# Kernel optimization log

Measured on AMD Instinct MI355X. Metric: run time of the kernel, lower is better.

## Reference

```python
import jax, jax.numpy as jnp
import numpy as np

NEURON_CDECAY = 0.5
NEURON_VDECAY = 0.75
NEURON_VTH = 0.5
SPIKE_WINDOW = 0.5


@jax.custom_vjp
def pseudo_spike(v):
    return (v > NEURON_VTH).astype(v.dtype)

def _ps_fwd(v):
    return pseudo_spike(v), v

def _ps_bwd(v, g):
    return (g * (jnp.abs(v - NEURON_VTH) < SPIKE_WINDOW).astype(g.dtype),)

pseudo_spike.defvjp(_ps_fwd, _ps_bwd)


def setup_inputs() -> dict:
    key = jax.random.key(0)
    ks = jax.random.split(key, 6)
    B, S, T, H, A = 4096, 256, 50, 256, 2
    # NCP mask with fanout=256 over 256 targets selects every target -> dense.
    x = jax.random.uniform(ks[0], (B, S, T), dtype=jnp.float32)
    w1 = jax.random.normal(ks[1], (S, H), dtype=jnp.float32)
    w2 = jax.random.normal(ks[2], (H, H), dtype=jnp.float32)
    w3 = jax.random.normal(ks[3], (H, H), dtype=jnp.float32)
    w4 = jax.random.normal(ks[4], (H, A), dtype=jnp.float32)
    b1 = jnp.zeros((H,), jnp.float32)
    b2 = jnp.zeros((H,), jnp.float32)
    b3 = jnp.zeros((H,), jnp.float32)
    b4 = jnp.zeros((A,), jnp.float32)
    return {"x": x, "w1": w1, "b1": b1, "w2": w2, "b2": b2,
            "w3": w3, "b3": b3, "w4": w4, "b4": b4, "batch_size": B}


def _lif(pre, W, b, u, v, s):
    # torch: linear(pre, weight=W.t(), bias=b) == pre @ W + b  (W is [src, tgt])
    cur = u * NEURON_CDECAY + pre @ W + b
    volt = v * NEURON_VDECAY * (1.0 - s) + cur
    spk = pseudo_spike(volt)
    return cur, volt, spk


def reference(x, w1, b1, w2, b2, w3, b3, w4, b4, batch_size):
    B = x.shape[0]
    T = x.shape[2]
    H1, H2, H3, A = w1.shape[1], w2.shape[1], w3.shape[1], w4.shape[1]
    z = lambda d: jnp.zeros((B, d), x.dtype)
    carry0 = (z(H1), z(H1), z(H1), z(H2), z(H2), z(H2),
              z(H3), z(H3), z(H3), z(A), z(A), z(A))
    xt = jnp.transpose(x, (2, 0, 1))  # [T, B, S]

    def step(carry, inp):
        u1, v1, s1, u2, v2, s2, u3, v3, s3, u4, v4, s4 = carry
        u1, v1, s1 = _lif(inp, w1, b1, u1, v1, s1)
        u2, v2, s2 = _lif(s1, w2, b2, u2, v2, s2)
        u3, v3, s3 = _lif(s2, w3, b3, u3, v3, s3)
        u4, v4, s4 = _lif(s3, w4, b4, u4, v4, s4)
        return (u1, v1, s1, u2, v2, s2, u3, v3, s3, u4, v4, s4), s4

    _, s4_all = jax.lax.scan(step, carry0, xt)  # [T, B, A]
    fc4_sumspike = jnp.sum(s4_all, axis=0) / T
    # faithful to the source: out is divided by batch_window a second time
    out = fc4_sumspike / T
    return out
```

## Files before the change

### kernel.cpp

```cpp
#include <hip/hip_runtime.h>

typedef unsigned short u16;
typedef unsigned int u32;

#define B_N 4096
#define S_N 256
#define T_N 50
#define H_N 256

#define W1F 0
#define W2F 65536
#define W3F 131072
#define W4F 196608
#define B1F 197120
#define B2F 197376
#define B3F 197632
#define B4F 197888
#define CVT_N 197890
#define FLAGI 198656

__device__ __forceinline__ float bf2f(u16 h) { return __uint_as_float(((u32)h) << 16); }
__device__ __forceinline__ u16 f2bf(float f) {
  u32 x = __float_as_uint(f);
  return (u16)((x + 0x7fffu + ((x >> 16) & 1u)) >> 16);
}
__device__ __forceinline__ float ld_f(const void* p, size_t i, int isbf) {
  return isbf ? bf2f(((const u16*)p)[i]) : ((const float*)p)[i];
}

__global__ void detect_dtype(const u16* __restrict__ x, int* __restrict__ flag) {
  __shared__ int cnt[256];
  int c = 0;
  for (int i = threadIdx.x; i < 4096; i += 256) c += (x[2 * i] <= 0x3F80u) ? 1 : 0;
  cnt[threadIdx.x] = c;
  __syncthreads();
  if (threadIdx.x == 0) {
    int tot = 0;
    for (int i = 0; i < 256; i++) tot += cnt[i];
    flag[0] = (tot > 3000) ? 1 : 0;
  }
}

__global__ void convert_inputs(const void* w1, const void* w2, const void* w3,
                               const void* w4, const void* b1, const void* b2,
                               const void* b3, const void* b4, float* __restrict__ ws) {
  const int isbf = ((const int*)ws)[FLAGI];
  int i = blockIdx.x * 256 + threadIdx.x;
  if (i >= CVT_N) return;
  float v;
  if (i < 196608) {
    const void* src = (i < 65536) ? w1 : (i < 131072 ? w2 : w3);
    const int j = i & 65535;
    const int k = j & 3, hp = (j >> 2) & 63, s = j >> 8;
    v = ld_f(src, (size_t)((s << 8) + (k << 6) + hp), isbf);
  } else if (i < 197120) v = ld_f(w4, (size_t)(i - W4F), isbf);
  else if (i < 197376) v = ld_f(b1, (size_t)(i - B1F), isbf);
  else if (i < 197632) v = ld_f(b2, (size_t)(i - B2F), isbf);
  else if (i < 197888) v = ld_f(b3, (size_t)(i - B3F), isbf);
  else v = ld_f(b4, (size_t)(i - B4F), isbf);
  ws[i] = v;
}

template <int OFF, int TN>
__device__ __forceinline__ void gemm_l1(const float4* __restrict__ wp,
                                        const float (*__restrict__ A)[52],
                                        int rdf, float (&acc)[13][4]) {
  const float4* ar0 = (const float4*)(&A[0][rdf]);
  float4 q0 = ar0[0], q1 = ar0[1], q2 = ar0[2], q3 = ar0[3];
  float4 wv = wp[0];
  for (int s = 0; s < S_N; s++) {
    const int sn = (s + 1) & 255;
    const float4* arn = (const float4*)(&A[sn][rdf]);
    float4 p0 = arn[0], p1 = arn[1], p2 = arn[2], p3 = arn[3];
    float4 wn = wp[(size_t)sn << 6];
    const float a[16] = {q0.x, q0.y, q0.z, q0.w, q1.x, q1.y, q1.z, q1.w,
                         q2.x, q2.y, q2.z, q2.w, q3.x, q3.y, q3.z, q3.w};
#pragma unroll
    for (int i = 0; i < TN; i++) {
      acc[i][0] = fmaf(a[OFF + i], wv.x, acc[i][0]);
      acc[i][1] = fmaf(a[OFF + i], wv.y, acc[i][1]);
      acc[i][2] = fmaf(a[OFF + i], wv.z, acc[i][2]);
      acc[i][3] = fmaf(a[OFF + i], wv.w, acc[i][3]);
    }
    q0 = p0; q1 = p1; q2 = p2; q3 = p3; wv = wn;
  }
}

template <int T0, int TN>
__device__ __forceinline__ void gemm_sp(const float4* __restrict__ wp,
                                        const float (*__restrict__ A)[52],
                                        float (&acc)[13][4]) {
  uint2 bv = *(const uint2*)(&A[0][50]);
  float4 wv = wp[0];
  for (int s = 0; s < S_N; s++) {
    const int sn = (s + 1) & 255;
    uint2 bn = *(const uint2*)(&A[sn][50]);
    float4 wn = wp[(size_t)sn << 6];
    const u32 bw0 = (u32)__builtin_amdgcn_readfirstlane((int)bv.x);
    const u32 bw1 = (u32)__builtin_amdgcn_readfirstlane((int)bv.y);
#pragma unroll
    for (int i = 0; i < TN; i++) {
      const int t = T0 + i;
      const u32 bw = (t < 32) ? bw0 : bw1;
      if (bw & (1u << (t & 31))) {
        acc[i][0] += wv.x; acc[i][1] += wv.y; acc[i][2] += wv.z; acc[i][3] += wv.w;
      }
    }
    bv = bn; wv = wn;
  }
}

__device__ __forceinline__ void lif_scan(float (*Af)[52], int tid, float bh) {
  float c[T_N];
  {
    const float4* rr = (const float4*)&Af[tid][0];
#pragma unroll
    for (int j = 0; j < 12; j++) {
      float4 v = rr[j];
      c[4 * j] = v.x; c[4 * j + 1] = v.y; c[4 * j + 2] = v.z; c[4 * j + 3] = v.w;
    }
    float2 v = *(const float2*)&Af[tid][48];
    c[48] = v.x; c[49] = v.y;
  }
  float uu = 0.f, vv = 0.f, ss = 0.f;
  u32 bw0 = 0u, bw1 = 0u;
#pragma unroll
  for (int t = 0; t < T_N; t++) {
    float cur = fmaf(uu, 0.5f, c[t]) + bh;
    float t1 = vv * 0.75f;
    float volt = fmaf(t1, 1.0f - ss, cur);
    bool sp = volt > 0.5f;
    if (t < 32) bw0 |= sp ? (1u << t) : 0u;
    else        bw1 |= sp ? (1u << (t - 32)) : 0u;
    uu = cur; vv = volt; ss = sp ? 1.0f : 0.0f;
  }
  ((u32*)&Af[tid][50])[0] = bw0;
  ((u32*)&Af[tid][50])[1] = bw1;
}

__global__ __launch_bounds__(256, 3) void snn_f32(
    const void* __restrict__ x, const float* __restrict__ ws, void* __restrict__ out) {
  __shared__ float Af[S_N][52];
  __shared__ float z4[T_N][2];

  const int b = blockIdx.x;
  const int tid = threadIdx.x;
  const int isbf = ((const int*)ws)[FLAGI];
  const int tq = tid >> 6;
  const int hp = tid & 63;
  const int t0 = (tq < 2) ? 13 * tq : 26 + 12 * (tq - 2);
  const int tn = (tq < 2) ? 13 : 12;
  const int rdf = 12 * tq;

  {
    const size_t base = ((size_t)b * S_N + tid) * T_N;
    if (isbf) {
      const u32* xr = (const u32*)((const u16*)x + base);
#pragma unroll
      for (int j = 0; j < 25; j++) {
        u32 d = xr[j];
        Af[tid][2 * j] = bf2f((u16)(d & 0xffffu));
        Af[tid][2 * j + 1] = bf2f((u16)(d >> 16));
      }
    } else {
      const float* xf = (const float*)x + base;
#pragma unroll
      for (int j = 0; j < 25; j++) {
        float2 d = *(const float2*)(xf + 2 * j);
        Af[tid][2 * j] = d.x;
        Af[tid][2 * j + 1] = d.y;
      }
    }
  }

  const int WOFF[3] = {W1F, W2F, W3F};
  const int BOFF[3] = {B1F, B2F, B3F};

  for (int l = 0; l < 3; l++) {
    __syncthreads();
    const float4* wp = (const float4*)(ws + WOFF[l]) + hp;

    float acc[13][4];
#pragma unroll
    for (int i = 0; i < 13; i++) {
#pragma unroll
      for (int k = 0; k < 4; k++) acc[i][k] = 0.0f;
    }

    if (l == 0) {
      if (tq == 0)      gemm_l1<0, 13>(wp, Af, 0, acc);
      else if (tq == 1) gemm_l1<1, 13>(wp, Af, 12, acc);
      else if (tq == 2) gemm_l1<2, 12>(wp, Af, 24, acc);
      else              gemm_l1<2, 12>(wp, Af, 36, acc);
    } else {
      if (tq == 0)      gemm_sp<0, 13>(wp, Af, acc);
      else if (tq == 1) gemm_sp<13, 13>(wp, Af, acc);
      else if (tq == 2) gemm_sp<26, 12>(wp, Af, acc);
      else              gemm_sp<38, 12>(wp, Af, acc);
    }
    __syncthreads();

#pragma unroll
    for (int i = 0; i < 13; i++) {
      if (i < tn) {
#pragma unroll
        for (int k = 0; k < 4; k++) Af[hp + 64 * k][t0 + i] = acc[i][k];
      }
    }
    __syncthreads();

    lif_scan(Af, tid, ws[BOFF[l] + tid]);
  }

  __syncthreads();
  if (tid < 2 * T_N) {
    const int t = tid >> 1, a = tid & 1;
    const int wd = t >> 5, bt = t & 31;
    float az = 0.f;
    const float* w4p = ws + W4F + a;
    for (int h = 0; h < H_N; h++) {
      const u32 bits = ((const u32*)&Af[h][50])[wd];
      const float m = (float)((bits >> bt) & 1u);
      az = fmaf(m, w4p[2 * h], az);
    }
    z4[t][a] = az;
  }
  __syncthreads();
  if (tid < 2) {
    const float bh = ws[B4F + tid];
    float uu = 0.f, vv = 0.f, ss = 0.f, sum = 0.f;
    for (int t = 0; t < T_N; t++) {
      float cur = fmaf(uu, 0.5f, z4[t][tid]) + bh;
      float t1 = vv * 0.75f;
      float volt = fmaf(t1, 1.0f - ss, cur);
      float sp = (volt > 0.5f) ? 1.0f : 0.0f;
      uu = cur; vv = volt; ss = sp;
      sum += sp;
    }
    float o = sum / 50.0f / 50.0f;
    if (isbf) ((u16*)out)[b * 2 + tid] = f2bf(o);
    else ((float*)out)[b * 2 + tid] = o;
  }
}

extern "C" void kernel_launch(void* const* d_in, const int* in_sizes, int n_in,
                              void* d_out, int out_size, void* d_ws, size_t ws_size,
                              hipStream_t stream) {
  const void* x  = d_in[0];
  const void* w1 = d_in[1];
  const void* b1 = d_in[2];
  const void* w2 = d_in[3];
  const void* b2 = d_in[4];
  const void* w3 = d_in[5];
  const void* b3 = d_in[6];
  const void* w4 = d_in[7];
  const void* b4 = d_in[8];

  float* ws = (float*)d_ws;
  int* flag = (int*)d_ws + FLAGI;

  detect_dtype<<<1, 256, 0, stream>>>((const u16*)x, flag);
  convert_inputs<<<(CVT_N + 255) / 256, 256, 0, stream>>>(w1, w2, w3, w4, b1, b2, b3, b4, ws);
  snn_f32<<<B_N, 256, 0, stream>>>(x, ws, d_out);
}
```

Baseline: 1.268 ms.

## Use branchless FMA masking in sparse GEMM, keep bf16 input packed, drop manual prefetch

Result: slower. 1.333 ms (+5.1%).

```diff
diff --git a/kernel.cpp b/kernel.cpp
--- a/kernel.cpp
+++ b/kernel.cpp
@@ -61,18 +61,36 @@
   ws[i] = v;
 }
 
+template <int T0, int TN, int WB>
+__device__ __forceinline__ void gemm_l1_bf(const float4* __restrict__ wp,
+                                           const float (*__restrict__ A)[52],
+                                           float (&acc)[13][4]) {
+  for (int s = 0; s < S_N; s++) {
+    const float4 wv = wp[(size_t)s << 6];
+    const uint2* ar = (const uint2*)((const u32*)&A[s][0] + WB);
+    const uint2 r0 = ar[0], r1 = ar[1], r2 = ar[2], r3 = ar[3];
+    const u32 wrd[8] = {r0.x, r0.y, r1.x, r1.y, r2.x, r2.y, r3.x, r3.y};
+#pragma unroll
+    for (int i = 0; i < TN; i++) {
+      const int p = T0 + i - 2 * WB;
+      const u32 w = wrd[p >> 1];
+      const float a = __uint_as_float((p & 1) ? (w & 0xffff0000u) : (w << 16));
+      acc[i][0] = fmaf(a, wv.x, acc[i][0]);
+      acc[i][1] = fmaf(a, wv.y, acc[i][1]);
+      acc[i][2] = fmaf(a, wv.z, acc[i][2]);
+      acc[i][3] = fmaf(a, wv.w, acc[i][3]);
+    }
+  }
+}
+
 template <int OFF, int TN>
-__device__ __forceinline__ void gemm_l1(const float4* __restrict__ wp,
-                                        const float (*__restrict__ A)[52],
-                                        int rdf, float (&acc)[13][4]) {
-  const float4* ar0 = (const float4*)(&A[0][rdf]);
-  float4 q0 = ar0[0], q1 = ar0[1], q2 = ar0[2], q3 = ar0[3];
-  float4 wv = wp[0];
+__device__ __forceinline__ void gemm_l1_f32(const float4* __restrict__ wp,
+                                            const float (*__restrict__ A)[52],
+                                            int rdf, float (&acc)[13][4]) {
   for (int s = 0; s < S_N; s++) {
-    const int sn = (s + 1) & 255;
-    const float4* arn = (const float4*)(&A[sn][rdf]);
-    float4 p0 = arn[0], p1 = arn[1], p2 = arn[2], p3 = arn[3];
-    float4 wn = wp[(size_t)sn << 6];
+    const float4 wv = wp[(size_t)s << 6];
+    const float4* ar = (const float4*)(&A[s][rdf]);
+    const float4 q0 = ar[0], q1 = ar[1], q2 = ar[2], q3 = ar[3];
     const float a[16] = {q0.x, q0.y, q0.z, q0.w, q1.x, q1.y, q1.z, q1.w,
                          q2.x, q2.y, q2.z, q2.w, q3.x, q3.y, q3.z, q3.w};
 #pragma unroll
@@ -82,7 +100,6 @@
       acc[i][2] = fmaf(a[OFF + i], wv.z, acc[i][2]);
       acc[i][3] = fmaf(a[OFF + i], wv.w, acc[i][3]);
     }
-    q0 = p0; q1 = p1; q2 = p2; q3 = p3; wv = wn;
   }
 }
 
@@ -90,23 +107,21 @@
 __device__ __forceinline__ void gemm_sp(const float4* __restrict__ wp,
                                         const float (*__restrict__ A)[52],
                                         float (&acc)[13][4]) {
-  uint2 bv = *(const uint2*)(&A[0][50]);
-  float4 wv = wp[0];
   for (int s = 0; s < S_N; s++) {
-    const int sn = (s + 1) & 255;
-    uint2 bn = *(const uint2*)(&A[sn][50]);
-    float4 wn = wp[(size_t)sn << 6];
-    const u32 bw0 = (u32)__builtin_amdgcn_readfirstlane((int)bv.x);
-    const u32 bw1 = (u32)__builtin_amdgcn_readfirstlane((int)bv.y);
+    const float4 wv = wp[(size_t)s << 6];
+    const uint2 bv = *(const uint2*)(&A[s][50]);
+    const u32 b0 = (u32)__builtin_amdgcn_readfirstlane((int)bv.x);
+    const u32 b1 = (u32)__builtin_amdgcn_readfirstlane((int)bv.y);
 #pragma unroll
     for (int i = 0; i < TN; i++) {
       const int t = T0 + i;
-      const u32 bw = (t < 32) ? bw0 : bw1;
-      if (bw & (1u << (t & 31))) {
-        acc[i][0] += wv.x; acc[i][1] += wv.y; acc[i][2] += wv.z; acc[i][3] += wv.w;
-      }
-    }
-    bv = bn; wv = wn;
+      const u32 bw = (t < 32) ? b0 : b1;
+      const float f = __uint_as_float((bw & (1u << (t & 31))) ? 0x3f800000u : 0u);
+      acc[i][0] = fmaf(f, wv.x, acc[i][0]);
+      acc[i][1] = fmaf(f, wv.y, acc[i][1]);
+      acc[i][2] = fmaf(f, wv.z, acc[i][2]);
+      acc[i][3] = fmaf(f, wv.w, acc[i][3]);
+    }
   }
 }
 
@@ -156,12 +171,9 @@
     const size_t base = ((size_t)b * S_N + tid) * T_N;
     if (isbf) {
       const u32* xr = (const u32*)((const u16*)x + base);
-#pragma unroll
-      for (int j = 0; j < 25; j++) {
-        u32 d = xr[j];
-        Af[tid][2 * j] = bf2f((u16)(d & 0xffffu));
-        Af[tid][2 * j + 1] = bf2f((u16)(d >> 16));
-      }
+      u32* dst = (u32*)&Af[tid][0];
+#pragma unroll
+      for (int j = 0; j < 25; j++) dst[j] = xr[j];
     } else {
       const float* xf = (const float*)x + base;
 #pragma unroll
@@ -188,10 +200,17 @@
     }
 
     if (l == 0) {
-      if (tq == 0)      gemm_l1<0, 13>(wp, Af, 0, acc);
-      else if (tq == 1) gemm_l1<1, 13>(wp, Af, 12, acc);
-      else if (tq == 2) gemm_l1<2, 12>(wp, Af, 24, acc);
-      else              gemm_l1<2, 12>(wp, Af, 36, acc);
+      if (isbf) {
+        if (tq == 0)      gemm_l1_bf<0, 13, 0>(wp, Af, acc);
+        else if (tq == 1) gemm_l1_bf<13, 13, 6>(wp, Af, acc);
+        else if (tq == 2) gemm_l1_bf<26, 12, 12>(wp, Af, acc);
+        else              gemm_l1_bf<38, 12, 18>(wp, Af, acc);
+      } else {
+        if (tq == 0)      gemm_l1_f32<0, 13>(wp, Af, 0, acc);
+        else if (tq == 1) gemm_l1_f32<1, 13>(wp, Af, 12, acc);
+        else if (tq == 2) gemm_l1_f32<2, 12>(wp, Af, 24, acc);
+        else              gemm_l1_f32<2, 12>(wp, Af, 36, acc);
+      }
     } else {
       if (tq == 0)      gemm_sp<0, 13>(wp, Af, acc);
       else if (tq == 1) gemm_sp<13, 13>(wp, Af, acc);
```
